# Kernel tuning notes

Hardware: AMD Instinct MI355X
Metric: run time of the kernel (lower is better)

Reference implementation:

```python
import jax, jax.numpy as jnp
import numpy as np

B, H, F, Z, T = 8192, 256, 128, 64, 43
STEPS = T - 3


def setup_inputs() -> dict:
    key = jax.random.key(0)
    ks = jax.random.split(key, 24)
    def nrm(k, shape, s=0.05):
        return (jax.random.normal(k, shape) * s).astype(jnp.float32)
    inp = {}
    inp["h_i"] = nrm(ks[0], (B, H), 1.0)                      # encoder context state
    t = jax.random.uniform(ks[1], (B, T)) * T                  # event timestamps, sorted
    inp["input_t"] = jnp.sort(t, axis=1).astype(jnp.float32)
    inp["eps_inf"] = jax.random.normal(ks[2], (STEPS, B, Z), dtype=jnp.float32)
    inp["eps_prior"] = jax.random.normal(ks[3], (STEPS, B, Z), dtype=jnp.float32)
    in_dim = Z + H + F
    inp["Wx"] = nrm(ks[4], (in_dim, 4 * H))
    inp["Wh"] = nrm(ks[5], (H, 4 * H))
    inp["b_lstm"] = jnp.zeros((4 * H,), jnp.float32)
    dims = [(H, F), (F, F), (F, F), (2 * H + 2 * F, Z), (Z, Z), (Z, Z), (2 * H + F, Z), (Z, Z), (Z, Z)]
    for i, (di, do) in enumerate(dims, 1):
        inp[f"w{i}"] = nrm(ks[5 + i], (di, do))
        inp[f"b{i}"] = jnp.zeros((do,), jnp.float32)
    inp["alpha"] = (jax.random.uniform(ks[20], (1, 1)) * 0.1).astype(jnp.float32)
    inp["beta"] = (jax.random.uniform(ks[21], (1, 1)) * 0.1).astype(jnp.float32)
    inp["mu0"] = (jax.random.uniform(ks[22], (1, 1)) * 0.1).astype(jnp.float32)
    return inp


def _forward(h_i, input_t, eps_inf, eps_prior, Wx, Wh, b_lstm,
             w1, b1, w2, b2, w3, b3, w4, b4, w5, b5, w6, b6, w7, b7, w8, b8, w9, b9,
             alpha, beta, mu0):
    batch = h_i.shape[0]
    idxs = jnp.arange(T)

    def dense(x, w, b):
        return jax.nn.relu(x @ w + b)

    def step(carry, xs):
        h, c, z_j, y_prev = carry
        e_i, e_p, j = xs
        # LSTM cell (Keras gate order i, f, c, o)
        x = jnp.concatenate([z_j, h_i, y_prev], axis=1)
        gates = x @ Wx + h @ Wh + b_lstm
        i_g, f_g, g_g, o_g = jnp.split(gates, 4, axis=1)
        c_new = jax.nn.sigmoid(f_g) * c + jax.nn.sigmoid(i_g) * jnp.tanh(g_g)
        h_new = jax.nn.sigmoid(o_g) * jnp.tanh(c_new)
        # Hawkes intensity over events strictly before current_time_index = j+3
        t_idx = j + 3
        t_cur = jnp.take(input_t, t_idx, axis=1)[:, None]          # [B,1]
        mask = idxs < t_idx                                         # [T]
        diff = jnp.where(mask[None, :], input_t - t_cur, -jnp.inf)
        trig = jnp.sum(jnp.exp(diff), axis=1, keepdims=True) * beta[0, 0]
        intensity = mu0[0, 0] + alpha[0, 0] * trig                  # [B,1]
        # original code gates state[1] (the cell state slot) with the intensity
        c_gated = intensity * c_new
        y = dense(dense(dense(h_new, w1, b1), w2, b2), w3, b3)
        # inference network (s_j = ungated c_new, mirroring the TF code)
        inf_in = jnp.concatenate([h_i, c_new, y, y_prev], axis=1)
        hz = dense(inf_in, w4, b4)
        mean_j = dense(hz, w5, b5)
        lv_j = dense(hz, w6, b6)
        z_new = mean_j + e_i * jnp.sqrt(jnp.exp(lv_j))
        # prior network
        pri_in = jnp.concatenate([h_i, c_new, y_prev], axis=1)
        hzp = dense(pri_in, w7, b7)
        mean_p = dense(hzp, w8, b8)
        lv_p = dense(hzp, w9, b9)
        z_p = mean_p + e_p * jnp.sqrt(jnp.exp(lv_p))
        return (h_new, c_gated, z_new, y), (y, mean_j, lv_j, z_new, z_p)

    carry0 = (jnp.zeros((batch, H), h_i.dtype), jnp.zeros((batch, H), h_i.dtype),
              jnp.zeros((batch, Z), h_i.dtype), jnp.zeros((batch, F), h_i.dtype))
    xs = (eps_inf, eps_prior, jnp.arange(STEPS))
    _, (ys, means, lvs, zs, zps) = jax.lax.scan(step, carry0, xs)
    # [STEPS,B,*] -> [B,STEPS,*]
    tr = lambda a: jnp.transpose(a, (1, 0, 2))
    return tr(ys), tr(means), tr(lvs), tr(zs), tr(zps)


def reference(h_i, input_t, eps_inf, eps_prior, Wx, Wh, b_lstm,
              w1, b1, w2, b2, w3, b3, w4, b4, w5, b5, w6, b6, w7, b7, w8, b8, w9, b9,
              alpha, beta, mu0):
    return _forward(h_i, input_t, eps_inf, eps_prior, Wx, Wh, b_lstm,
                    w1, b1, w2, b2, w3, b3, w4, b4, w5, b5, w6, b6, w7, b7, w8, b8, w9, b9,
                    alpha, beta, mu0)
```

## Files before the change

kernel.cpp:

```cpp
#include <hip/hip_runtime.h>


#define BDIM  8192
#define HDIM  256
#define FDIM  128
#define ZDIM  64
#define TDIM  43
#define STEPS 40

typedef __attribute__((ext_vector_type(8))) __bf16 bf16x8;
typedef __attribute__((ext_vector_type(4))) float  f32x4;

#define ACT_STRIDE 3248
#define C_Z   0
#define C_Y0  64
#define C_Y1  192
#define C_H0  320
#define C_H1  576
#define C_C   832
#define C_T0  1088
#define C_T1  1216
#define C_HZ  1344
#define C_HZP 1408
#define C_B4  1472
#define C_B7  1536

#define PW_GS  0u
#define PW_GHI 458752u
#define PW_W1  720896u
#define PW_W2  753664u
#define PW_W3  770048u
#define PW_W4S 786432u
#define PW_W4H 819200u
#define PW_W5  835584u
#define PW_W6  839680u
#define PW_W7S 843776u
#define PW_W7H 868352u
#define PW_W8  884736u
#define PW_W9  888832u

#define SB() __builtin_amdgcn_sched_barrier(0)

__device__ __forceinline__ int act_off(int row, int col) {
  return row * ACT_STRIDE + ((row >> 3) << 4) + (col << 1);
}
__device__ __forceinline__ f32x4 mfma16(bf16x8 a, bf16x8 b, f32x4 c) {
  return __builtin_amdgcn_mfma_f32_16x16x32_bf16(a, b, c, 0, 0, 0);
}
__device__ __forceinline__ float sigm(float x) { return 1.f / (1.f + __expf(-x)); }
__device__ __forceinline__ float tanh_f(float x) {
  float t = __expf(-2.f * fabsf(x));
  float r = (1.f - t) / (1.f + t);
  return x < 0.f ? -r : r;
}
__device__ __forceinline__ void wg_barrier() {
  asm volatile("s_waitcnt lgkmcnt(0)" ::: "memory");
  __builtin_amdgcn_s_barrier();
  __builtin_amdgcn_sched_barrier(0);
}
__device__ __forceinline__ bf16x8 aread(const unsigned char* actb, int mt, int col,
                                        int lane) {
  return *(const bf16x8*)(actb + act_off(mt * 16 + (lane & 15), col + ((lane >> 4) << 3)));
}
__device__ __forceinline__ void st16(unsigned char* actb, int col, int mt, int rsub,
                                     f32x4 v, float bv) {
#pragma unroll
  for (int r = 0; r < 4; ++r)
    *(__bf16*)(actb + act_off(mt * 16 + rsub + r, col)) = (__bf16)fmaxf(v[r] + bv, 0.f);
}
__device__ __forceinline__ unsigned int pk2(float a, float b) {
  union { __bf16 h; unsigned short u; } x, y;
  x.h = (__bf16)a; y.h = (__bf16)b;
  return (unsigned int)x.u | ((unsigned int)y.u << 16);
}
__device__ __forceinline__ float upkf(unsigned int u, int hi) {
  union { unsigned int i; float f; } c;
  c.i = hi ? (u & 0xffff0000u) : (u << 16);
  return c.f;
}

struct PSeg { const float* p; int row0; int len; };

__global__ __launch_bounds__(256) void pack_w(PSeg s0, PSeg s1, PSeg s2,
                                              int K, int N, __bf16* __restrict__ dst) {
  int f = blockIdx.x * 256 + threadIdx.x;
  int KT = K >> 5;
  int total = KT * (N >> 4) * 64;
  if (f >= total) return;
  int lane = f & 63;
  int tile = f >> 6;
  int kt = tile % KT;
  int nt = tile / KT;
  int k0 = kt * 32 + ((lane >> 4) << 3);
  int n = (nt << 4) + (lane & 15);
  bf16x8 v;
#pragma unroll
  for (int j = 0; j < 8; ++j) {
    int k = k0 + j;
    const float* src;
    int r;
    if (k < s0.len) { src = s0.p; r = s0.row0 + k; }
    else if (k < s0.len + s1.len) { src = s1.p; r = s1.row0 + (k - s0.len); }
    else { src = s2.p; r = s2.row0 + (k - s0.len - s1.len); }
    v[j] = (__bf16)src[(size_t)r * N + n];
  }
  *(bf16x8*)(dst + (size_t)f * 8) = v;
}

struct Params {
  const float *h_i, *input_t, *eps_inf, *eps_prior;
  const float *b_lstm, *b1, *b2, *b3, *b4, *b5, *b6, *b7, *b8, *b9;
  const float *alpha, *beta, *mu0;
  const __bf16* wpack;
  float* out;
};

#define LDK(t, ktv)                                                         \
  do {                                                                      \
    _Pragma("unroll") for (int g = 0; g < 4; ++g) wb[t][g] =                \
        wgs[((size_t)(g * 16 + w) * 14 + (ktv)) * 64 + lane];               \
  } while (0)

__global__ __launch_bounds__(1024, 4) void decoder_main(Params p) {
  __shared__ __align__(16) unsigned char act[32 * ACT_STRIDE];
  __shared__ float fbuf[2048];
  __shared__ float inten[STEPS * 32];

  const int tid = threadIdx.x;
  const int w = tid >> 6;
  const int lane = tid & 63;
  const int ln16 = lane & 15;
  const int rsub = (lane >> 4) << 2;
  const int r0 = blockIdx.x * 32;

  for (int i = tid; i < (32 * ACT_STRIDE) / 4; i += 1024) ((unsigned int*)act)[i] = 0u;
  __syncthreads();
  for (int i = tid; i < 32 * 256; i += 1024) {
    int row = i >> 8, col = i & 255;
    *(__bf16*)(act + act_off(row, C_C + col)) =
        (__bf16)p.h_i[(size_t)(r0 + row) * HDIM + col];
  }
  {
    float ab = p.alpha[0] * p.beta[0], mu = p.mu0[0];
    for (int t = tid; t < 32 * STEPS; t += 1024) {
      int row = t & 31, j = t >> 5;
      const float* tp = p.input_t + (size_t)(r0 + row) * TDIM;
      float tc = tp[j + 3];
      float s = 0.f;
      for (int idx = 0; idx < j + 3; ++idx) s += __expf(tp[idx] - tc);
      inten[j * 32 + row] = mu + ab * s;
    }
  }
  __syncthreads();

  const __bf16* W = p.wpack;
  const bf16x8* wgs = (const bf16x8*)(W + PW_GS);
  const bf16x8* wghi = (const bf16x8*)(W + PW_GHI);
  const bf16x8* w1p = (const bf16x8*)(W + PW_W1);
  const bf16x8* w2p = (const bf16x8*)(W + PW_W2);
  const bf16x8* w3p = (const bf16x8*)(W + PW_W3);
  const bf16x8* w4s = (const bf16x8*)(W + PW_W4S);
  const bf16x8* w4h = (const bf16x8*)(W + PW_W4H);
  const bf16x8* w5p = (const bf16x8*)(W + PW_W5);
  const bf16x8* w6p = (const bf16x8*)(W + PW_W6);
  const bf16x8* w7s = (const bf16x8*)(W + PW_W7S);
  const bf16x8* w7h = (const bf16x8*)(W + PW_W7H);
  const bf16x8* w8p = (const bf16x8*)(W + PW_W8);
  const bf16x8* w9p = (const bf16x8*)(W + PW_W9);

  uint2 gbp[4][2];
  {
    f32x4 g[4][2] = {};
#pragma unroll
    for (int kt = 0; kt < 8; ++kt) {
      bf16x8 a0 = aread(act, 0, C_C + kt * 32, lane);
      bf16x8 a1 = aread(act, 1, C_C + kt * 32, lane);
#pragma unroll
      for (int gg = 0; gg < 4; ++gg) {
        bf16x8 b = wghi[((size_t)(gg * 16 + w) * 8 + kt) * 64 + lane];
        g[gg][0] = mfma16(a0, b, g[gg][0]);
        g[gg][1] = mfma16(a1, b, g[gg][1]);
      }
    }
#pragma unroll
    for (int gg = 0; gg < 4; ++gg) {
      float bv = p.b_lstm[gg * 256 + w * 16 + ln16];
#pragma unroll
      for (int mt = 0; mt < 2; ++mt) {
        gbp[gg][mt].x = pk2(g[gg][mt][0] + bv, g[gg][mt][1] + bv);
        gbp[gg][mt].y = pk2(g[gg][mt][2] + bv, g[gg][mt][3] + bv);
      }
    }
  }
  {
    int n = w & 3, mt = (w >> 2) & 1;
    const bf16x8* wp = (w < 8) ? w4h : w7h;
    const float* bb = (w < 8) ? p.b4 : p.b7;
    int cb = (w < 8) ? C_B4 : C_B7;
    f32x4 v = {};
#pragma unroll
    for (int kt = 0; kt < 8; ++kt)
      v = mfma16(aread(act, mt, C_C + kt * 32, lane),
                 wp[(size_t)(n * 8 + kt) * 64 + lane], v);
    float bv = bb[n * 16 + ln16];
#pragma unroll
    for (int r = 0; r < 4; ++r)
      *(__bf16*)(act + act_off(mt * 16 + rsub + r, cb + n * 16 + ln16)) =
          (__bf16)(v[r] + bv);
  }
  f32x4 c_st[2] = {};

  float bv1 = 0.f, bv2 = 0.f, bv3 = 0.f, bmA = 0.f, blA = 0.f;
  {
    int n = w & 3;
    if (w < 8) {
      bv1 = p.b1[w * 16 + ln16];
      bv2 = p.b2[w * 16 + ln16];
      bv3 = p.b3[w * 16 + ln16];
      bmA = p.b5[n * 16 + ln16];
      blA = p.b6[n * 16 + ln16];
    } else {
      bmA = p.b8[n * 16 + ln16];
      blA = p.b9[n * 16 + ln16];
    }
  }
  __syncthreads();

  float* outy = p.out;
  float* outm = p.out + (size_t)BDIM * STEPS * FDIM;
  float* outl = outm + (size_t)BDIM * STEPS * ZDIM;
  float* outz = outl + (size_t)BDIM * STEPS * ZDIM;
  float* outzp = outz + (size_t)BDIM * STEPS * ZDIM;

  bf16x8 wb[3][4];
  LDK(0, 0);
  LDK(1, 1);
  LDK(2, 2);
  SB();

  for (int j = 0; j < STEPS; ++j) {
    const int yW = (j & 1) ? C_Y1 : C_Y0, yR = (j & 1) ? C_Y0 : C_Y1;
    const int hW = (j & 1) ? C_H1 : C_H0, hR = (j & 1) ? C_H0 : C_H1;

    {
      f32x4 acc[4][2] = {};
#pragma unroll
      for (int kt = 0; kt < 14; ++kt) {
        int col = (kt < 2) ? (C_Z + kt * 32)
                           : (kt < 6) ? (yR + (kt - 2) * 32) : (hR + (kt - 6) * 32);
        bf16x8 a0 = aread(act, 0, col, lane);
        bf16x8 a1 = aread(act, 1, col, lane);
        const int s = kt % 3;
#pragma unroll
        for (int g = 0; g < 4; ++g) {
          acc[g][0] = mfma16(a0, wb[s][g], acc[g][0]);
          acc[g][1] = mfma16(a1, wb[s][g], acc[g][1]);
        }
        if (kt + 3 < 14) LDK(s, kt + 3);
        SB();
      }
#pragma unroll
      for (int mt = 0; mt < 2; ++mt) {
#pragma unroll
        for (int r = 0; r < 4; ++r) {
          int row = mt * 16 + rsub + r;
          unsigned int ui = (r < 2) ? gbp[0][mt].x : gbp[0][mt].y;
          unsigned int uf = (r < 2) ? gbp[1][mt].x : gbp[1][mt].y;
          unsigned int ug = (r < 2) ? gbp[2][mt].x : gbp[2][mt].y;
          unsigned int uo = (r < 2) ? gbp[3][mt].x : gbp[3][mt].y;
          float ig = sigm(acc[0][mt][r] + upkf(ui, r & 1));
          float fg = sigm(acc[1][mt][r] + upkf(uf, r & 1));
          float gg = tanh_f(acc[2][mt][r] + upkf(ug, r & 1));
          float og = sigm(acc[3][mt][r] + upkf(uo, r & 1));
          float cn = fg * c_st[mt][r] + ig * gg;
          float hn = og * tanh_f(cn);
          c_st[mt][r] = inten[j * 32 + row] * cn;
          *(__bf16*)(act + act_off(row, C_C + w * 16 + ln16)) = (__bf16)cn;
          *(__bf16*)(act + act_off(row, hW + w * 16 + ln16)) = (__bf16)hn;
        }
      }
    }
    wg_barrier();

    if (w < 8) {
      bf16x8 wf[8];
#pragma unroll
      for (int kt = 0; kt < 8; ++kt) wf[kt] = w1p[(size_t)(w * 8 + kt) * 64 + lane];
      SB();
      f32x4 a0 = {}, a1 = {};
#pragma unroll
      for (int kt = 0; kt < 8; ++kt) {
        a0 = mfma16(aread(act, 0, hW + kt * 32, lane), wf[kt], a0);
        a1 = mfma16(aread(act, 1, hW + kt * 32, lane), wf[kt], a1);
      }
      st16(act, C_T0 + w * 16 + ln16, 0, rsub, a0, bv1);
      st16(act, C_T0 + w * 16 + ln16, 1, rsub, a1, bv1);
    } else {
      int n = w & 3, mt = (w >> 2) & 1;
      bf16x8 wf[12];
#pragma unroll
      for (int kt = 0; kt < 12; ++kt) wf[kt] = w7s[(size_t)(n * 12 + kt) * 64 + lane];
      SB();
      f32x4 v = {};
#pragma unroll
      for (int kt = 0; kt < 12; ++kt) {
        int col = (kt < 8) ? (C_C + kt * 32) : (yR + (kt - 8) * 32);
        v = mfma16(aread(act, mt, col, lane), wf[kt], v);
      }
#pragma unroll
      for (int r = 0; r < 4; ++r) {
        int row = mt * 16 + rsub + r;
        float s = v[r] + (float)*(const __bf16*)(act + act_off(row, C_B7 + n * 16 + ln16));
        *(__bf16*)(act + act_off(row, C_HZP + n * 16 + ln16)) = (__bf16)fmaxf(s, 0.f);
      }
    }
    wg_barrier();

    if (w < 8) {
      bf16x8 wf[4];
#pragma unroll
      for (int kt = 0; kt < 4; ++kt) wf[kt] = w2p[(size_t)(w * 4 + kt) * 64 + lane];
      SB();
      f32x4 a0 = {}, a1 = {};
#pragma unroll
      for (int kt = 0; kt < 4; ++kt) {
        a0 = mfma16(aread(act, 0, C_T0 + kt * 32, lane), wf[kt], a0);
        a1 = mfma16(aread(act, 1, C_T0 + kt * 32, lane), wf[kt], a1);
      }
      st16(act, C_T1 + w * 16 + ln16, 0, rsub, a0, bv2);
      st16(act, C_T1 + w * 16 + ln16, 1, rsub, a1, bv2);
    } else {
      int n = w & 3, mt = (w >> 2) & 1;
      bf16x8 wm[2], wl[2];
      float ep[4];
#pragma unroll
      for (int kt = 0; kt < 2; ++kt) {
        wm[kt] = w8p[(size_t)(n * 2 + kt) * 64 + lane];
        wl[kt] = w9p[(size_t)(n * 2 + kt) * 64 + lane];
      }
#pragma unroll
      for (int r = 0; r < 4; ++r)
        ep[r] = __builtin_nontemporal_load(
            p.eps_prior + ((size_t)j * BDIM + r0 + mt * 16 + rsub + r) * ZDIM +
            n * 16 + ln16);
      SB();
      f32x4 vm = {}, vl = {};
#pragma unroll
      for (int kt = 0; kt < 2; ++kt) {
        bf16x8 a = aread(act, mt, C_HZP + kt * 32, lane);
        vm = mfma16(a, wm[kt], vm);
        vl = mfma16(a, wl[kt], vl);
      }
#pragma unroll
      for (int r = 0; r < 4; ++r) {
        int row = mt * 16 + rsub + r, col = n * 16 + ln16;
        float mp = fmaxf(vm[r] + bmA, 0.f), lp = fmaxf(vl[r] + blA, 0.f);
        float zp = mp + ep[r] * __expf(0.5f * lp);
        __builtin_nontemporal_store(
            zp, outzp + ((size_t)(r0 + row) * STEPS + j) * ZDIM + col);
      }
    }
    wg_barrier();

    if (w < 8) {
      bf16x8 wf[4];
#pragma unroll
      for (int kt = 0; kt < 4; ++kt) wf[kt] = w3p[(size_t)(w * 4 + kt) * 64 + lane];
      SB();
      f32x4 a0 = {}, a1 = {};
#pragma unroll
      for (int kt = 0; kt < 4; ++kt) {
        a0 = mfma16(aread(act, 0, C_T1 + kt * 32, lane), wf[kt], a0);
        a1 = mfma16(aread(act, 1, C_T1 + kt * 32, lane), wf[kt], a1);
      }
#pragma unroll
      for (int mt = 0; mt < 2; ++mt) {
        f32x4 vv = mt ? a1 : a0;
#pragma unroll
        for (int r = 0; r < 4; ++r) {
          int row = mt * 16 + rsub + r;
          float yv = fmaxf(vv[r] + bv3, 0.f);
          *(__bf16*)(act + act_off(row, yW + w * 16 + ln16)) = (__bf16)yv;
          __builtin_nontemporal_store(
              yv, outy + ((size_t)(r0 + row) * STEPS + j) * FDIM + w * 16 + ln16);
        }
      }
    } else {
      int a = w - 8, n = a & 3, mt = a >> 2;
      bf16x8 wf[12];
#pragma unroll
      for (int kk = 0; kk < 12; ++kk) {
        int kt = (kk < 8) ? kk : (kk + 4);
        wf[kk] = w4s[(size_t)(n * 16 + kt) * 64 + lane];
      }
      SB();
      f32x4 v = {};
#pragma unroll
      for (int kk = 0; kk < 12; ++kk) {
        int col = (kk < 8) ? (C_C + kk * 32) : (yR + (kk - 8) * 32);
        v = mfma16(aread(act, mt, col, lane), wf[kk], v);
      }
#pragma unroll
      for (int r = 0; r < 4; ++r)
        fbuf[(mt * 16 + rsub + r) * 64 + n * 16 + ln16] = v[r];
    }
    wg_barrier();

    LDK(0, 0);
    LDK(1, 1);
    LDK(2, 2);
    SB();
    if (w < 8) {
      int n = w & 3, mt = w >> 2;
      bf16x8 wf[4];
#pragma unroll
      for (int kt = 8; kt < 12; ++kt) wf[kt - 8] = w4s[(size_t)(n * 16 + kt) * 64 + lane];
      SB();
      f32x4 v = {};
#pragma unroll
      for (int kt = 8; kt < 12; ++kt)
        v = mfma16(aread(act, mt, yW + (kt - 8) * 32, lane), wf[kt - 8], v);
#pragma unroll
      for (int r = 0; r < 4; ++r) {
        int row = mt * 16 + rsub + r, cc = n * 16 + ln16;
        float s = v[r] + fbuf[row * 64 + cc] +
                  (float)*(const __bf16*)(act + act_off(row, C_B4 + cc));
        *(__bf16*)(act + act_off(row, C_HZ + cc)) = (__bf16)fmaxf(s, 0.f);
      }
    }
    wg_barrier();

    if (w < 8) {
      int n = w & 3, mt = w >> 2;
      bf16x8 wm[2], wl[2];
      float ei[4];
#pragma unroll
      for (int kt = 0; kt < 2; ++kt) {
        wm[kt] = w5p[(size_t)(n * 2 + kt) * 64 + lane];
        wl[kt] = w6p[(size_t)(n * 2 + kt) * 64 + lane];
      }
#pragma unroll
      for (int r = 0; r < 4; ++r)
        ei[r] = __builtin_nontemporal_load(
            p.eps_inf + ((size_t)j * BDIM + r0 + mt * 16 + rsub + r) * ZDIM +
            n * 16 + ln16);
      SB();
      f32x4 vm = {}, vl = {};
#pragma unroll
      for (int kt = 0; kt < 2; ++kt) {
        bf16x8 a = aread(act, mt, C_HZ + kt * 32, lane);
        vm = mfma16(a, wm[kt], vm);
        vl = mfma16(a, wl[kt], vl);
      }
#pragma unroll
      for (int r = 0; r < 4; ++r) {
        int row = mt * 16 + rsub + r, col = n * 16 + ln16;
        float m = fmaxf(vm[r] + bmA, 0.f), l = fmaxf(vl[r] + blA, 0.f);
        float zn = m + ei[r] * __expf(0.5f * l);
        size_t ob = ((size_t)(r0 + row) * STEPS + j) * ZDIM + col;
        __builtin_nontemporal_store(m, outm + ob);
        __builtin_nontemporal_store(l, outl + ob);
        __builtin_nontemporal_store(zn, outz + ob);
        *(__bf16*)(act + act_off(row, C_Z + col)) = (__bf16)zn;
      }
    }
    wg_barrier();
  }
}

extern "C" void kernel_launch(void* const* d_in, const int* in_sizes, int n_in,
                              void* d_out, int out_size, void* d_ws, size_t ws_size,
                              hipStream_t stream) {
  const float* h_i = (const float*)d_in[0];
  const float* input_t = (const float*)d_in[1];
  const float* eps_inf = (const float*)d_in[2];
  const float* eps_prior = (const float*)d_in[3];
  const float* Wx = (const float*)d_in[4];
  const float* Wh = (const float*)d_in[5];
  const float* b_lstm = (const float*)d_in[6];
  const float* w1 = (const float*)d_in[7];  const float* b1 = (const float*)d_in[8];
  const float* w2 = (const float*)d_in[9];  const float* b2 = (const float*)d_in[10];
  const float* w3 = (const float*)d_in[11]; const float* b3 = (const float*)d_in[12];
  const float* w4 = (const float*)d_in[13]; const float* b4 = (const float*)d_in[14];
  const float* w5 = (const float*)d_in[15]; const float* b5 = (const float*)d_in[16];
  const float* w6 = (const float*)d_in[17]; const float* b6 = (const float*)d_in[18];
  const float* w7 = (const float*)d_in[19]; const float* b7 = (const float*)d_in[20];
  const float* w8 = (const float*)d_in[21]; const float* b8 = (const float*)d_in[22];
  const float* w9 = (const float*)d_in[23]; const float* b9 = (const float*)d_in[24];
  const float* alpha = (const float*)d_in[25];
  const float* beta = (const float*)d_in[26];
  const float* mu0 = (const float*)d_in[27];
  __bf16* ws = (__bf16*)d_ws;

  auto S = [](const float* ptr, int row0, int len) {
    PSeg s; s.p = ptr; s.row0 = row0; s.len = len; return s;
  };
  PSeg Zs; Zs.p = nullptr; Zs.row0 = 0; Zs.len = 0;
  auto L = [&](PSeg a, PSeg b, PSeg c, int K, int N, unsigned off) {
    int total = (K / 32) * (N / 16) * 64;
    pack_w<<<(total + 255) / 256, 256, 0, stream>>>(a, b, c, K, N, ws + off);
  };
  L(S(Wx, 0, 64), S(Wx, 320, 128), S(Wh, 0, 256), 448, 1024, PW_GS);
  L(S(Wx, 64, 256), Zs, Zs, 256, 1024, PW_GHI);
  L(S(w1, 0, 256), Zs, Zs, 256, 128, PW_W1);
  L(S(w2, 0, 128), Zs, Zs, 128, 128, PW_W2);
  L(S(w3, 0, 128), Zs, Zs, 128, 128, PW_W3);
  L(S(w4, 256, 512), Zs, Zs, 512, 64, PW_W4S);
  L(S(w4, 0, 256), Zs, Zs, 256, 64, PW_W4H);
  L(S(w5, 0, 64), Zs, Zs, 64, 64, PW_W5);
  L(S(w6, 0, 64), Zs, Zs, 64, 64, PW_W6);
  L(S(w7, 256, 384), Zs, Zs, 384, 64, PW_W7S);
  L(S(w7, 0, 256), Zs, Zs, 256, 64, PW_W7H);
  L(S(w8, 0, 64), Zs, Zs, 64, 64, PW_W8);
  L(S(w9, 0, 64), Zs, Zs, 64, 64, PW_W9);

  Params p;
  p.h_i = h_i; p.input_t = input_t; p.eps_inf = eps_inf; p.eps_prior = eps_prior;
  p.b_lstm = b_lstm; p.b1 = b1; p.b2 = b2; p.b3 = b3; p.b4 = b4; p.b5 = b5;
  p.b6 = b6; p.b7 = b7; p.b8 = b8; p.b9 = b9;
  p.alpha = alpha; p.beta = beta; p.mu0 = mu0;
  p.wpack = ws;
  p.out = (float*)d_out;

  decoder_main<<<256, 1024, 0, stream>>>(p);
}
```

Measured before the change: 2.426 ms.

## Halve workgroup to 8 waves with doubled per-wave work and explicit vmcnt prefetch

```diff
diff --git a/kernel.cpp b/kernel.cpp
--- a/kernel.cpp
+++ b/kernel.cpp
@@ -10,6 +10,7 @@
 
 typedef __attribute__((ext_vector_type(8))) __bf16 bf16x8;
 typedef __attribute__((ext_vector_type(4))) float  f32x4;
+typedef __attribute__((ext_vector_type(4))) int    i32x4;
 
 #define ACT_STRIDE 3248
 #define C_Z   0
@@ -40,6 +41,11 @@
 #define PW_W9  888832u
 
 #define SB() __builtin_amdgcn_sched_barrier(0)
+#define VMW(N)                                             \
+  do {                                                     \
+    asm volatile("s_waitcnt vmcnt(" #N ")" ::: "memory");  \
+    SB();                                                  \
+  } while (0)
 
 __device__ __forceinline__ int act_off(int row, int col) {
   return row * ACT_STRIDE + ((row >> 3) << 4) + (col << 1);
@@ -57,6 +63,16 @@
   asm volatile("s_waitcnt lgkmcnt(0)" ::: "memory");
   __builtin_amdgcn_s_barrier();
   __builtin_amdgcn_sched_barrier(0);
+}
+__device__ __forceinline__ bf16x8 gld(const bf16x8* p) {
+  i32x4 r;
+  asm volatile("global_load_dwordx4 %0, %1, off" : "=v"(r) : "v"(p));
+  return __builtin_bit_cast(bf16x8, r);
+}
+__device__ __forceinline__ float gldf(const float* p) {
+  float r;
+  asm volatile("global_load_dword %0, %1, off" : "=v"(r) : "v"(p));
+  return r;
 }
 __device__ __forceinline__ bf16x8 aread(const unsigned char* actb, int mt, int col,
                                         int lane) {
@@ -115,13 +131,18 @@
   float* out;
 };
 
-#define LDK(t, ktv)                                                         \
-  do {                                                                      \
-    _Pragma("unroll") for (int g = 0; g < 4; ++g) wb[t][g] =                \
-        wgs[((size_t)(g * 16 + w) * 14 + (ktv)) * 64 + lane];               \
-  } while (0)
-
-__global__ __launch_bounds__(1024, 4) void decoder_main(Params p) {
+__device__ __forceinline__ void issue_gchunk(bf16x8 (&wf)[8], const bf16x8* wgs,
+                                             int w, int lane, int kt) {
+#pragma unroll
+  for (int g = 0; g < 4; ++g)
+#pragma unroll
+    for (int t = 0; t < 2; ++t)
+      wf[g * 2 + t] =
+          gld(wgs + ((size_t)((g * 16 + w * 2 + t) * 14 + kt) << 6) + lane);
+}
+
+__global__ __launch_bounds__(512) __attribute__((amdgpu_waves_per_eu(2, 2)))
+void decoder_main(Params p) {
   __shared__ __align__(16) unsigned char act[32 * ACT_STRIDE];
   __shared__ float fbuf[2048];
   __shared__ float inten[STEPS * 32];
@@ -133,16 +154,16 @@
   const int rsub = (lane >> 4) << 2;
   const int r0 = blockIdx.x * 32;
 
-  for (int i = tid; i < (32 * ACT_STRIDE) / 4; i += 1024) ((unsigned int*)act)[i] = 0u;
+  for (int i = tid; i < (32 * ACT_STRIDE) / 4; i += 512) ((unsigned int*)act)[i] = 0u;
   __syncthreads();
-  for (int i = tid; i < 32 * 256; i += 1024) {
+  for (int i = tid; i < 32 * 256; i += 512) {
     int row = i >> 8, col = i & 255;
     *(__bf16*)(act + act_off(row, C_C + col)) =
         (__bf16)p.h_i[(size_t)(r0 + row) * HDIM + col];
   }
   {
     float ab = p.alpha[0] * p.beta[0], mu = p.mu0[0];
-    for (int t = tid; t < 32 * STEPS; t += 1024) {
+    for (int t = tid; t < 32 * STEPS; t += 512) {
       int row = t & 31, j = t >> 5;
       const float* tp = p.input_t + (size_t)(r0 + row) * TDIM;
       float tc = tp[j + 3];
@@ -168,62 +189,56 @@
   const bf16x8* w8p = (const bf16x8*)(W + PW_W8);
   const bf16x8* w9p = (const bf16x8*)(W + PW_W9);
 
-  uint2 gbp[4][2];
+  uint2 gbp[4][2][2];
   {
-    f32x4 g[4][2] = {};
+    f32x4 g4[4][2][2] = {};
 #pragma unroll
     for (int kt = 0; kt < 8; ++kt) {
       bf16x8 a0 = aread(act, 0, C_C + kt * 32, lane);
       bf16x8 a1 = aread(act, 1, C_C + kt * 32, lane);
 #pragma unroll
-      for (int gg = 0; gg < 4; ++gg) {
-        bf16x8 b = wghi[((size_t)(gg * 16 + w) * 8 + kt) * 64 + lane];
-        g[gg][0] = mfma16(a0, b, g[gg][0]);
-        g[gg][1] = mfma16(a1, b, g[gg][1]);
-      }
-    }
-#pragma unroll
-    for (int gg = 0; gg < 4; ++gg) {
-      float bv = p.b_lstm[gg * 256 + w * 16 + ln16];
-#pragma unroll
-      for (int mt = 0; mt < 2; ++mt) {
-        gbp[gg][mt].x = pk2(g[gg][mt][0] + bv, g[gg][mt][1] + bv);
-        gbp[gg][mt].y = pk2(g[gg][mt][2] + bv, g[gg][mt][3] + bv);
-      }
-    }
+      for (int g = 0; g < 4; ++g)
+#pragma unroll
+        for (int t = 0; t < 2; ++t) {
+          bf16x8 b = wghi[((size_t)((g * 16 + w * 2 + t) * 8 + kt)) * 64 + lane];
+          g4[g][t][0] = mfma16(a0, b, g4[g][t][0]);
+          g4[g][t][1] = mfma16(a1, b, g4[g][t][1]);
+        }
+    }
+#pragma unroll
+    for (int g = 0; g < 4; ++g)
+#pragma unroll
+      for (int t = 0; t < 2; ++t) {
+        float bv = p.b_lstm[g * 256 + (w * 2 + t) * 16 + ln16];
+#pragma unroll
+        for (int mt = 0; mt < 2; ++mt) {
+          gbp[g][t][mt].x = pk2(g4[g][t][mt][0] + bv, g4[g][t][mt][1] + bv);
+          gbp[g][t][mt].y = pk2(g4[g][t][mt][2] + bv, g4[g][t][mt][3] + bv);
+        }
+      }
   }
   {
-    int n = w & 3, mt = (w >> 2) & 1;
-    const bf16x8* wp = (w < 8) ? w4h : w7h;
-    const float* bb = (w < 8) ? p.b4 : p.b7;
-    int cb = (w < 8) ? C_B4 : C_B7;
-    f32x4 v = {};
-#pragma unroll
-    for (int kt = 0; kt < 8; ++kt)
-      v = mfma16(aread(act, mt, C_C + kt * 32, lane),
-                 wp[(size_t)(n * 8 + kt) * 64 + lane], v);
-    float bv = bb[n * 16 + ln16];
-#pragma unroll
-    for (int r = 0; r < 4; ++r)
-      *(__bf16*)(act + act_off(mt * 16 + rsub + r, cb + n * 16 + ln16)) =
-          (__bf16)(v[r] + bv);
+    int n = w & 3, mt = w >> 2;
+    f32x4 v4 = {}, v7 = {};
+#pragma unroll
+    for (int kt = 0; kt < 8; ++kt) {
+      bf16x8 a = aread(act, mt, C_C + kt * 32, lane);
+      v4 = mfma16(a, w4h[(size_t)(n * 8 + kt) * 64 + lane], v4);
+      v7 = mfma16(a, w7h[(size_t)(n * 8 + kt) * 64 + lane], v7);
+    }
+    float b4v = p.b4[n * 16 + ln16], b7v = p.b7[n * 16 + ln16];
+#pragma unroll
+    for (int r = 0; r < 4; ++r) {
+      int row = mt * 16 + rsub + r;
+      *(__bf16*)(act + act_off(row, C_B4 + n * 16 + ln16)) = (__bf16)(v4[r] + b4v);
+      *(__bf16*)(act + act_off(row, C_B7 + n * 16 + ln16)) = (__bf16)(v7[r] + b7v);
+    }
   }
-  f32x4 c_st[2] = {};
-
-  float bv1 = 0.f, bv2 = 0.f, bv3 = 0.f, bmA = 0.f, blA = 0.f;
-  {
-    int n = w & 3;
-    if (w < 8) {
-      bv1 = p.b1[w * 16 + ln16];
-      bv2 = p.b2[w * 16 + ln16];
-      bv3 = p.b3[w * 16 + ln16];
-      bmA = p.b5[n * 16 + ln16];
-      blA = p.b6[n * 16 + ln16];
-    } else {
-      bmA = p.b8[n * 16 + ln16];
-      blA = p.b9[n * 16 + ln16];
-    }
-  }
+  f32x4 c_st[2][2] = {};
+  const int nw = w & 3, mw = w >> 2;
+  float bv1 = p.b1[w * 16 + ln16], bv2 = p.b2[w * 16 + ln16], bv3 = p.b3[w * 16 + ln16];
+  float b5v = p.b5[nw * 16 + ln16], b6v = p.b6[nw * 16 + ln16];
+  float b8v = p.b8[nw * 16 + ln16], b9v = p.b9[nw * 16 + ln16];
   __syncthreads();
 
   float* outy = p.out;
@@ -232,129 +247,137 @@
   float* outz = outl + (size_t)BDIM * STEPS * ZDIM;
   float* outzp = outz + (size_t)BDIM * STEPS * ZDIM;
 
-  bf16x8 wb[3][4];
-  LDK(0, 0);
-  LDK(1, 1);
-  LDK(2, 2);
-  SB();
+  bf16x8 wgbuf[2][8];
+  issue_gchunk(wgbuf[0], wgs, w, lane, 0);
+  issue_gchunk(wgbuf[1], wgs, w, lane, 1);
 
   for (int j = 0; j < STEPS; ++j) {
     const int yW = (j & 1) ? C_Y1 : C_Y0, yR = (j & 1) ? C_Y0 : C_Y1;
     const int hW = (j & 1) ? C_H1 : C_H0, hR = (j & 1) ? C_H0 : C_H1;
 
     {
-      f32x4 acc[4][2] = {};
+      f32x4 acc[4][2][2];
+#pragma unroll
+      for (int g = 0; g < 4; ++g)
+#pragma unroll
+        for (int t = 0; t < 2; ++t)
+#pragma unroll
+          for (int mt = 0; mt < 2; ++mt) {
+            acc[g][t][mt][0] = upkf(gbp[g][t][mt].x, 0);
+            acc[g][t][mt][1] = upkf(gbp[g][t][mt].x, 1);
+            acc[g][t][mt][2] = upkf(gbp[g][t][mt].y, 0);
+            acc[g][t][mt][3] = upkf(gbp[g][t][mt].y, 1);
+          }
 #pragma unroll
       for (int kt = 0; kt < 14; ++kt) {
+        if (kt < 13) { VMW(8); } else { VMW(0); }
         int col = (kt < 2) ? (C_Z + kt * 32)
                            : (kt < 6) ? (yR + (kt - 2) * 32) : (hR + (kt - 6) * 32);
         bf16x8 a0 = aread(act, 0, col, lane);
         bf16x8 a1 = aread(act, 1, col, lane);
-        const int s = kt % 3;
-#pragma unroll
-        for (int g = 0; g < 4; ++g) {
-          acc[g][0] = mfma16(a0, wb[s][g], acc[g][0]);
-          acc[g][1] = mfma16(a1, wb[s][g], acc[g][1]);
-        }
-        if (kt + 3 < 14) LDK(s, kt + 3);
+#pragma unroll
+        for (int g = 0; g < 4; ++g)
+#pragma unroll
+          for (int t = 0; t < 2; ++t) {
+            acc[g][t][0] = mfma16(a0, wgbuf[kt & 1][g * 2 + t], acc[g][t][0]);
+            acc[g][t][1] = mfma16(a1, wgbuf[kt & 1][g * 2 + t], acc[g][t][1]);
+          }
         SB();
-      }
-#pragma unroll
-      for (int mt = 0; mt < 2; ++mt) {
-#pragma unroll
-        for (int r = 0; r < 4; ++r) {
-          int row = mt * 16 + rsub + r;
-          unsigned int ui = (r < 2) ? gbp[0][mt].x : gbp[0][mt].y;
-          unsigned int uf = (r < 2) ? gbp[1][mt].x : gbp[1][mt].y;
-          unsigned int ug = (r < 2) ? gbp[2][mt].x : gbp[2][mt].y;
-          unsigned int uo = (r < 2) ? gbp[3][mt].x : gbp[3][mt].y;
-          float ig = sigm(acc[0][mt][r] + upkf(ui, r & 1));
-          float fg = sigm(acc[1][mt][r] + upkf(uf, r & 1));
-          float gg = tanh_f(acc[2][mt][r] + upkf(ug, r & 1));
-          float og = sigm(acc[3][mt][r] + upkf(uo, r & 1));
-          float cn = fg * c_st[mt][r] + ig * gg;
-          float hn = og * tanh_f(cn);
-          c_st[mt][r] = inten[j * 32 + row] * cn;
-          *(__bf16*)(act + act_off(row, C_C + w * 16 + ln16)) = (__bf16)cn;
-          *(__bf16*)(act + act_off(row, hW + w * 16 + ln16)) = (__bf16)hn;
-        }
+        if (kt + 2 < 14) issue_gchunk(wgbuf[kt & 1], wgs, w, lane, kt + 2);
+      }
+#pragma unroll
+      for (int t = 0; t < 2; ++t) {
+        int colc = (w * 2 + t) * 16 + ln16;
+#pragma unroll
+        for (int mt = 0; mt < 2; ++mt)
+#pragma unroll
+          for (int r = 0; r < 4; ++r) {
+            int row = mt * 16 + rsub + r;
+            float ig = sigm(acc[0][t][mt][r]);
+            float fg = sigm(acc[1][t][mt][r]);
+            float gg = tanh_f(acc[2][t][mt][r]);
+            float og = sigm(acc[3][t][mt][r]);
+            float cn = fg * c_st[t][mt][r] + ig * gg;
+            float hn = og * tanh_f(cn);
+            c_st[t][mt][r] = inten[j * 32 + row] * cn;
+            *(__bf16*)(act + act_off(row, C_C + colc)) = (__bf16)cn;
+            *(__bf16*)(act + act_off(row, hW + colc)) = (__bf16)hn;
+          }
       }
     }
     wg_barrier();
 
-    if (w < 8) {
-      bf16x8 wf[8];
-#pragma unroll
-      for (int kt = 0; kt < 8; ++kt) wf[kt] = w1p[(size_t)(w * 8 + kt) * 64 + lane];
-      SB();
+    {
+      bf16x8 wy[8];
+#pragma unroll
+      for (int kt = 0; kt < 8; ++kt)
+        wy[kt] = gld(w1p + (size_t)(w * 8 + kt) * 64 + lane);
+      bf16x8 wpr[12];
+#pragma unroll
+      for (int kt = 0; kt < 12; ++kt)
+        wpr[kt] = gld(w7s + (size_t)(nw * 12 + kt) * 64 + lane);
+      VMW(12);
       f32x4 a0 = {}, a1 = {};
 #pragma unroll
       for (int kt = 0; kt < 8; ++kt) {
-        a0 = mfma16(aread(act, 0, hW + kt * 32, lane), wf[kt], a0);
-        a1 = mfma16(aread(act, 1, hW + kt * 32, lane), wf[kt], a1);
+        a0 = mfma16(aread(act, 0, hW + kt * 32, lane), wy[kt], a0);
+        a1 = mfma16(aread(act, 1, hW + kt * 32, lane), wy[kt], a1);
       }
       st16(act, C_T0 + w * 16 + ln16, 0, rsub, a0, bv1);
       st16(act, C_T0 + w * 16 + ln16, 1, rsub, a1, bv1);
-    } else {
-      int n = w & 3, mt = (w >> 2) & 1;
-      bf16x8 wf[12];
-#pragma unroll
-      for (int kt = 0; kt < 12; ++kt) wf[kt] = w7s[(size_t)(n * 12 + kt) * 64 + lane];
-      SB();
+      VMW(0);
       f32x4 v = {};
 #pragma unroll
       for (int kt = 0; kt < 12; ++kt) {
         int col = (kt < 8) ? (C_C + kt * 32) : (yR + (kt - 8) * 32);
-        v = mfma16(aread(act, mt, col, lane), wf[kt], v);
+        v = mfma16(aread(act, mw, col, lane), wpr[kt], v);
       }
 #pragma unroll
       for (int r = 0; r < 4; ++r) {
-        int row = mt * 16 + rsub + r;
-        float s = v[r] + (float)*(const __bf16*)(act + act_off(row, C_B7 + n * 16 + ln16));
-        *(__bf16*)(act + act_off(row, C_HZP + n * 16 + ln16)) = (__bf16)fmaxf(s, 0.f);
+        int row = mw * 16 + rsub + r;
+        float s = v[r] + (float)*(const __bf16*)(act + act_off(row, C_B7 + nw * 16 + ln16));
+        *(__bf16*)(act + act_off(row, C_HZP + nw * 16 + ln16)) = (__bf16)fmaxf(s, 0.f);
       }
     }
     wg_barrier();
 
-    if (w < 8) {
-      bf16x8 wf[4];
-#pragma unroll
-      for (int kt = 0; kt < 4; ++kt) wf[kt] = w2p[(size_t)(w * 4 + kt) * 64 + lane];
-      SB();
+    {
+      bf16x8 w2f[4];
+#pragma unroll
+      for (int kt = 0; kt < 4; ++kt)
+        w2f[kt] = gld(w2p + (size_t)(w * 4 + kt) * 64 + lane);
+      bf16x8 w8f[2], w9f[2];
+#pragma unroll
+      for (int kt = 0; kt < 2; ++kt) {
+        w8f[kt] = gld(w8p + (size_t)(nw * 2 + kt) * 64 + lane);
+        w9f[kt] = gld(w9p + (size_t)(nw * 2 + kt) * 64 + lane);
+      }
+      float ep[4];
+#pragma unroll
+      for (int r = 0; r < 4; ++r)
+        ep[r] = gldf(p.eps_prior + ((size_t)j * BDIM + r0 + mw * 16 + rsub + r) * ZDIM +
+                     nw * 16 + ln16);
+      VMW(8);
       f32x4 a0 = {}, a1 = {};
 #pragma unroll
       for (int kt = 0; kt < 4; ++kt) {
-        a0 = mfma16(aread(act, 0, C_T0 + kt * 32, lane), wf[kt], a0);
-        a1 = mfma16(aread(act, 1, C_T0 + kt * 32, lane), wf[kt], a1);
+        a0 = mfma16(aread(act, 0, C_T0 + kt * 32, lane), w2f[kt], a0);
+        a1 = mfma16(aread(act, 1, C_T0 + kt * 32, lane), w2f[kt], a1);
       }
       st16(act, C_T1 + w * 16 + ln16, 0, rsub, a0, bv2);
       st16(act, C_T1 + w * 16 + ln16, 1, rsub, a1, bv2);
-    } else {
-      int n = w & 3, mt = (w >> 2) & 1;
-      bf16x8 wm[2], wl[2];
-      float ep[4];
+      VMW(0);
+      f32x4 vm = {}, vl = {};
 #pragma unroll
       for (int kt = 0; kt < 2; ++kt) {
-        wm[kt] = w8p[(size_t)(n * 2 + kt) * 64 + lane];
-        wl[kt] = w9p[(size_t)(n * 2 + kt) * 64 + lane];
-      }
-#pragma unroll
-      for (int r = 0; r < 4; ++r)
-        ep[r] = __builtin_nontemporal_load(
-            p.eps_prior + ((size_t)j * BDIM + r0 + mt * 16 + rsub + r) * ZDIM +
-            n * 16 + ln16);
-      SB();
-      f32x4 vm = {}, vl = {};
-#pragma unroll
-      for (int kt = 0; kt < 2; ++kt) {
-        bf16x8 a = aread(act, mt, C_HZP + kt * 32, lane);
-        vm = mfma16(a, wm[kt], vm);
-        vl = mfma16(a, wl[kt], vl);
+        bf16x8 a = aread(act, mw, C_HZP + kt * 32, lane);
+        vm = mfma16(a, w8f[kt], vm);
+        vl = mfma16(a, w9f[kt], vl);
       }
 #pragma unroll
       for (int r = 0; r < 4; ++r) {
-        int row = mt * 16 + rsub + r, col = n * 16 + ln16;
-        float mp = fmaxf(vm[r] + bmA, 0.f), lp = fmaxf(vl[r] + blA, 0.f);
+        int row = mw * 16 + rsub + r, col = nw * 16 + ln16;
+        float mp = fmaxf(vm[r] + b8v, 0.f), lp = fmaxf(vl[r] + b9v, 0.f);
         float zp = mp + ep[r] * __expf(0.5f * lp);
         __builtin_nontemporal_store(
             zp, outzp + ((size_t)(r0 + row) * STEPS + j) * ZDIM + col);
@@ -362,16 +385,23 @@
     }
     wg_barrier();
 
-    if (w < 8) {
-      bf16x8 wf[4];
-#pragma unroll
-      for (int kt = 0; kt < 4; ++kt) wf[kt] = w3p[(size_t)(w * 4 + kt) * 64 + lane];
-      SB();
+    {
+      bf16x8 w3f[4];
+#pragma unroll
+      for (int kt = 0; kt < 4; ++kt)
+        w3f[kt] = gld(w3p + (size_t)(w * 4 + kt) * 64 + lane);
+      bf16x8 w4c[12];
+#pragma unroll
+      for (int kk = 0; kk < 12; ++kk) {
+        int kt = (kk < 8) ? kk : (kk + 4);
+        w4c[kk] = gld(w4s + (size_t)(nw * 16 + kt) * 64 + lane);
+      }
+      VMW(12);
       f32x4 a0 = {}, a1 = {};
 #pragma unroll
       for (int kt = 0; kt < 4; ++kt) {
-        a0 = mfma16(aread(act, 0, C_T1 + kt * 32, lane), wf[kt], a0);
-        a1 = mfma16(aread(act, 1, C_T1 + kt * 32, lane), wf[kt], a1);
+        a0 = mfma16(aread(act, 0, C_T1 + kt * 32, lane), w3f[kt], a0);
+        a1 = mfma16(aread(act, 1, C_T1 + kt * 32, lane), w3f[kt], a1);
       }
 #pragma unroll
       for (int mt = 0; mt < 2; ++mt) {
@@ -385,44 +415,45 @@
               yv, outy + ((size_t)(r0 + row) * STEPS + j) * FDIM + w * 16 + ln16);
         }
       }
-    } else {
-      int a = w - 8, n = a & 3, mt = a >> 2;
-      bf16x8 wf[12];
-#pragma unroll
-      for (int kk = 0; kk < 12; ++kk) {
-        int kt = (kk < 8) ? kk : (kk + 4);
-        wf[kk] = w4s[(size_t)(n * 16 + kt) * 64 + lane];
-      }
-      SB();
+      VMW(0);
       f32x4 v = {};
 #pragma unroll
       for (int kk = 0; kk < 12; ++kk) {
         int col = (kk < 8) ? (C_C + kk * 32) : (yR + (kk - 8) * 32);
-        v = mfma16(aread(act, mt, col, lane), wf[kk], v);
+        v = mfma16(aread(act, mw, col, lane), w4c[kk], v);
       }
 #pragma unroll
       for (int r = 0; r < 4; ++r)
-        fbuf[(mt * 16 + rsub + r) * 64 + n * 16 + ln16] = v[r];
+        fbuf[(mw * 16 + rsub + r) * 64 + nw * 16 + ln16] = v[r];
     }
     wg_barrier();
 
-    LDK(0, 0);
-    LDK(1, 1);
-    LDK(2, 2);
-    SB();
-    if (w < 8) {
-      int n = w & 3, mt = w >> 2;
-      bf16x8 wf[4];
-#pragma unroll
-      for (int kt = 8; kt < 12; ++kt) wf[kt - 8] = w4s[(size_t)(n * 16 + kt) * 64 + lane];
-      SB();
+    bf16x8 w5f[2], w6f[2];
+    float ei[4];
+    {
+      bf16x8 w4y[4];
+#pragma unroll
+      for (int kt = 8; kt < 12; ++kt)
+        w4y[kt - 8] = gld(w4s + (size_t)(nw * 16 + kt) * 64 + lane);
+#pragma unroll
+      for (int kt = 0; kt < 2; ++kt) {
+        w5f[kt] = gld(w5p + (size_t)(nw * 2 + kt) * 64 + lane);
+        w6f[kt] = gld(w6p + (size_t)(nw * 2 + kt) * 64 + lane);
+      }
+#pragma unroll
+      for (int r = 0; r < 4; ++r)
+        ei[r] = gldf(p.eps_inf + ((size_t)j * BDIM + r0 + mw * 16 + rsub + r) * ZDIM +
+                     nw * 16 + ln16);
+      issue_gchunk(wgbuf[0], wgs, w, lane, 0);
+      issue_gchunk(wgbuf[1], wgs, w, lane, 1);
+      VMW(24);
       f32x4 v = {};
 #pragma unroll
       for (int kt = 8; kt < 12; ++kt)
-        v = mfma16(aread(act, mt, yW + (kt - 8) * 32, lane), wf[kt - 8], v);
+        v = mfma16(aread(act, mw, yW + (kt - 8) * 32, lane), w4y[kt - 8], v);
 #pragma unroll
       for (int r = 0; r < 4; ++r) {
-        int row = mt * 16 + rsub + r, cc = n * 16 + ln16;
+        int row = mw * 16 + rsub + r, cc = nw * 16 + ln16;
         float s = v[r] + fbuf[row * 64 + cc] +
                   (float)*(const __bf16*)(act + act_off(row, C_B4 + cc));
         *(__bf16*)(act + act_off(row, C_HZ + cc)) = (__bf16)fmaxf(s, 0.f);
@@ -430,32 +461,19 @@
     }
     wg_barrier();
 
-    if (w < 8) {
-      int n = w & 3, mt = w >> 2;
-      bf16x8 wm[2], wl[2];
-      float ei[4];
+    {
+      VMW(16);
+      f32x4 vm = {}, vl = {};
 #pragma unroll
       for (int kt = 0; kt < 2; ++kt) {
-        wm[kt] = w5p[(size_t)(n * 2 + kt) * 64 + lane];
-        wl[kt] = w6p[(size_t)(n * 2 + kt) * 64 + lane];
-      }
-#pragma unroll
-      for (int r = 0; r < 4; ++r)
-        ei[r] = __builtin_nontemporal_load(
-            p.eps_inf + ((size_t)j * BDIM + r0 + mt * 16 + rsub + r) * ZDIM +
-            n * 16 + ln16);
-      SB();
-      f32x4 vm = {}, vl = {};
-#pragma unroll
-      for (int kt = 0; kt < 2; ++kt) {
-        bf16x8 a = aread(act, mt, C_HZ + kt * 32, lane);
-        vm = mfma16(a, wm[kt], vm);
-        vl = mfma16(a, wl[kt], vl);
+        bf16x8 a = aread(act, mw, C_HZ + kt * 32, lane);
+        vm = mfma16(a, w5f[kt], vm);
+        vl = mfma16(a, w6f[kt], vl);
       }
 #pragma unroll
       for (int r = 0; r < 4; ++r) {
-        int row = mt * 16 + rsub + r, col = n * 16 + ln16;
-        float m = fmaxf(vm[r] + bmA, 0.f), l = fmaxf(vl[r] + blA, 0.f);
+        int row = mw * 16 + rsub + r, col = nw * 16 + ln16;
+        float m = fmaxf(vm[r] + b5v, 0.f), l = fmaxf(vl[r] + b6v, 0.f);
         float zn = m + ei[r] * __expf(0.5f * l);
         size_t ob = ((size_t)(r0 + row) * STEPS + j) * ZDIM + col;
         __builtin_nontemporal_store(m, outm + ob);
@@ -522,5 +540,5 @@
   p.wpack = ws;
   p.out = (float*)d_out;
 
-  decoder_main<<<256, 1024, 0, stream>>>(p);
-}
+  decoder_main<<<256, 512, 0, stream>>>(p);
+}
```

Result: slower. 3.269 ms (+34.8%).
